# Optimization experiments

Hardware: AMD Instinct MI355X
Metric: run time of the kernel (lower is better)

The kernel has to match this reference:

```python
import jax, jax.numpy as jnp
import numpy as np

NUM_HEADS = 12


def _qkv_split(x, qkv_w, num_heads):
    B, N, C = x.shape
    hd = C // num_heads
    qkv = (x @ qkv_w).reshape(B, N, 3, num_heads, hd)
    qkv = jnp.transpose(qkv, (2, 0, 3, 1, 4))  # [3, B, H, N, hd]
    return qkv[0], qkv[1], qkv[2]


def setup_inputs() -> dict:
    key = jax.random.key(0)
    k1, k2, k3, k4 = jax.random.split(key, 4)
    B, N, C = 8, 1024, 768
    s = 0.02
    return {
        "x1": jax.random.normal(k1, (B, N, C), dtype=jnp.float32),
        "x2": jax.random.normal(k2, (B, N, C), dtype=jnp.float32),
        "qkv_w": jax.random.normal(k3, (C, 3 * C), dtype=jnp.float32) * s,
        "proj_w": jax.random.normal(k4, (C, C), dtype=jnp.float32) * s,
        "proj_b": jnp.zeros((C,), dtype=jnp.float32),
    }


def reference(x1, x2, qkv_w, proj_w, proj_b):
    B, N, C = x1.shape
    H = NUM_HEADS
    hd = C // H
    scale = hd ** (-0.5)

    q, k, v = _qkv_split(x1, qkv_w, H)    # each [B, H, N, hd]
    q2, k2, v2 = _qkv_split(x2, qkv_w, H)

    # self-attention branch: q attends to k/v (from x1)
    attn1 = jax.nn.softmax(jnp.einsum('bhqd,bhkd->bhqk', q, k) * scale, axis=-1)
    o1 = jnp.einsum('bhqk,bhkd->bhqd', attn1, v)

    # cross-attention branch: same q attends to k2/v2 (from x2)
    attn2 = jax.nn.softmax(jnp.einsum('bhqd,bhkd->bhqk', q, k2) * scale, axis=-1)
    o2 = jnp.einsum('bhqk,bhkd->bhqd', attn2, v2)

    o1 = jnp.transpose(o1, (0, 2, 1, 3)).reshape(B, N, C) @ proj_w + proj_b
    o2 = jnp.transpose(o2, (0, 2, 1, 3)).reshape(B, N, C) @ proj_w + proj_b
    return (o1, o2)
```

## Files before the change

kernel.cpp:

```cpp
#include <hip/hip_runtime.h>
#include <hip/hip_bf16.h>

#define N_ 1024
#define C_ 768
#define H_ 12

typedef unsigned short u16;
typedef __attribute__((ext_vector_type(8))) short bf16x8;
typedef __attribute__((ext_vector_type(4))) float f32x4;
typedef __attribute__((ext_vector_type(16))) float f32x16;

#define MFMA16(a, b, c) __builtin_amdgcn_mfma_f32_16x16x32_bf16(a, b, c, 0, 0, 0)
#define MFMA32(a, b, c) __builtin_amdgcn_mfma_f32_32x32x16_bf16(a, b, c, 0, 0, 0)

#define GLDS16(gp, lp) __builtin_amdgcn_global_load_lds(                     \
    (const __attribute__((address_space(1))) void*)(gp),                     \
    (__attribute__((address_space(3))) void*)(lp), 16, 0, 0)

__device__ __forceinline__ u16 f2bu(float x) {
    unsigned u = __float_as_uint(x);
    unsigned r = (u + 0x7fffu + ((u >> 16) & 1u)) >> 16;
    return (u16)r;
}

__device__ __forceinline__ unsigned cvtpk(float a, float b) {
    unsigned d;
    asm("v_cvt_pk_bf16_f32 %0, %1, %2" : "=v"(d) : "v"(a), "v"(b));
    return d;
}

__global__ __launch_bounds__(256) void cvt_x(
    const float* __restrict__ x1, const float* __restrict__ x2,
    u16* __restrict__ d1, u16* __restrict__ d2)
{
    const size_t G = 786432;
    for (size_t i = (size_t)blockIdx.x * 256 + threadIdx.x; i < 2 * G;
         i += (size_t)gridDim.x * 256) {
        const float* src = (i < G) ? x1 : x2;
        u16* dst = (i < G) ? d1 : d2;
        size_t g = (i < G) ? i : i - G;
        float4 f0 = ((const float4*)src)[g * 2];
        float4 f1 = ((const float4*)src)[g * 2 + 1];
        ushort4 lo, hi;
        lo.x = f2bu(f0.x); lo.y = f2bu(f0.y); lo.z = f2bu(f0.z); lo.w = f2bu(f0.w);
        hi.x = f2bu(f1.x); hi.y = f2bu(f1.y); hi.z = f2bu(f1.z); hi.w = f2bu(f1.w);
        ((ushort4*)dst)[g * 2] = lo;
        ((ushort4*)dst)[g * 2 + 1] = hi;
    }
}

__global__ __launch_bounds__(256) void tr_cvt(
    const float* __restrict__ W, u16* __restrict__ WT, int R, int CC)
{
    __shared__ float t[32][33];
    const int tx = threadIdx.x & 31, ty = threadIdx.x >> 5;
    const int c0 = blockIdx.x * 32, r0 = blockIdx.y * 32;
#pragma unroll
    for (int i = 0; i < 4; ++i) {
        int r = ty + i * 8;
        t[r][tx] = W[(size_t)(r0 + r) * CC + c0 + tx];
    }
    __syncthreads();
#pragma unroll
    for (int i = 0; i < 4; ++i) {
        int c = ty + i * 8;
        WT[(size_t)(c0 + c) * R + r0 + tx] = f2bu(t[tx][c]);
    }
}

__global__ __launch_bounds__(256, 4) void qkv_gemm(
    const u16* __restrict__ A1, const u16* __restrict__ A2,
    const u16* __restrict__ BT, u16* __restrict__ qd,
    u16* __restrict__ k1d, u16* __restrict__ k2d,
    u16* __restrict__ vt1d, u16* __restrict__ vt2d)
{
    __shared__ u16 As[3][128 * 32];
    __shared__ u16 Bs[3][128 * 32];
    const int tid = threadIdx.x;
    const int w = tid >> 6, lane = tid & 63;
    const int c31 = lane & 31, h = lane >> 5;
    const int wm = w >> 1, wn = w & 1;
    const int id = blockIdx.x;
    const int xcd = id & 7, j = id >> 3;
    const int by = xcd * 8 + j / 30;
    const int bx = j % 30;
    const bool first = bx < 18;
    const u16* A = first ? A1 : A2;
    const int row0 = by * 128;
    const int nc0 = first ? bx * 128 : 768 + (bx - 18) * 128;

    f32x16 acc[2][2];
#pragma unroll
    for (int i = 0; i < 2; ++i)
#pragma unroll
        for (int jj = 0; jj < 2; ++jj)
#pragma unroll
            for (int e = 0; e < 16; ++e) acc[i][jj][e] = 0.f;

    int aoff[2], boff[2];
    char *adst[2], *bdst[2];
#pragma unroll
    for (int i = 0; i < 2; ++i) {
        int L = (i * 256 + tid) * 16;
        int row = L >> 6;
        int slot = (L >> 4) & 3;
        int sw = (slot ^ ((row >> 1) & 3)) * 8;
        aoff[i] = (row0 + row) * C_ + sw;
        boff[i] = (nc0 + row) * C_ + sw;
        adst[i] = (char*)&As[0][0] + i * 4096 + w * 1024;
        bdst[i] = (char*)&Bs[0][0] + i * 4096 + w * 1024;
    }
    auto stage = [&](int buf, int k0) {
#pragma unroll
        for (int i = 0; i < 2; ++i) {
            GLDS16(A + aoff[i] + k0, adst[i] + buf * 8192);
            GLDS16(BT + boff[i] + k0, bdst[i] + buf * 8192);
        }
    };

    const int ra0 = wm * 64 + c31, ra1 = ra0 + 32;
    const int rb0 = wn * 64 + c31, rb1 = rb0 + 32;

    stage(0, 0);
    stage(1, 32);
    int buf = 0;
    for (int kt = 0; kt < 24; ++kt) {
        if (kt < 23) { asm volatile("s_waitcnt vmcnt(4)" ::: "memory"); }
        else         { asm volatile("s_waitcnt vmcnt(0)" ::: "memory"); }
        __builtin_amdgcn_s_barrier();
        if (kt + 2 < 24) {
            int nb = buf + 2; if (nb >= 3) nb -= 3;
            stage(nb, (kt + 2) * 32);
        }
        const char* abase = (const char*)&As[0][0] + buf * 8192;
        const char* bbase = (const char*)&Bs[0][0] + buf * 8192;
#pragma unroll
        for (int kh = 0; kh < 2; ++kh) {
            bf16x8 a0 = *(const bf16x8*)(abase + ra0 * 64 + (((h + 2 * kh) ^ ((ra0 >> 1) & 3)) * 16));
            bf16x8 a1 = *(const bf16x8*)(abase + ra1 * 64 + (((h + 2 * kh) ^ ((ra1 >> 1) & 3)) * 16));
            bf16x8 b0 = *(const bf16x8*)(bbase + rb0 * 64 + (((h + 2 * kh) ^ ((rb0 >> 1) & 3)) * 16));
            bf16x8 b1 = *(const bf16x8*)(bbase + rb1 * 64 + (((h + 2 * kh) ^ ((rb1 >> 1) & 3)) * 16));
            acc[0][0] = MFMA32(a0, b0, acc[0][0]);
            acc[0][1] = MFMA32(a0, b1, acc[0][1]);
            acc[1][0] = MFMA32(a1, b0, acc[1][0]);
            acc[1][1] = MFMA32(a1, b1, acc[1][1]);
        }
        if (++buf >= 3) buf = 0;
    }

    u16* kd  = first ? k1d : k2d;
    u16* vtd = first ? vt1d : vt2d;
    const int abscol = nc0 + wn * 64;
    const int sec = abscol / C_;
    const int hh = (abscol % C_) >> 6;
    const float scl = (sec == 0) ? 0.180336877f : 1.0f;
#pragma unroll
    for (int mt = 0; mt < 2; ++mt)
#pragma unroll
        for (int nt = 0; nt < 2; ++nt)
#pragma unroll
            for (int r = 0; r < 16; ++r) {
                int row = row0 + wm * 64 + mt * 32 + (r & 3) + 8 * (r >> 2) + 4 * h;
                int b = row >> 10, n = row & 1023;
                int d = nt * 32 + c31;
                u16 val = f2bu(acc[mt][nt][r] * scl);
                size_t bh = (size_t)(b * H_ + hh);
                if (sec == 0)      qd[(bh * N_ + n) * 64 + d] = val;
                else if (sec == 1) kd[(bh * N_ + n) * 64 + d] = val;
                else {
                    int nprm = (n & ~63) | (((n & 15) << 2) | ((n >> 4) & 3));
                    vtd[(bh * 64 + d) * N_ + nprm] = val;
                }
            }
}

__global__ __launch_bounds__(256, 4) void proj_gemm(
    const u16* __restrict__ A1, const u16* __restrict__ A2,
    const u16* __restrict__ BT, const float* __restrict__ bias,
    float* __restrict__ out)
{
    __shared__ u16 As[3][128 * 32];
    __shared__ u16 Bs[3][128 * 32];
    const int tid = threadIdx.x;
    const int w = tid >> 6, lane = tid & 63;
    const int c31 = lane & 31, h = lane >> 5;
    const int wm = w >> 1, wn = w & 1;
    const int sel = blockIdx.y >> 6;
    const u16* A = sel ? A2 : A1;
    float* op = out + (size_t)sel * 8192 * C_;
    const int row0 = (blockIdx.y & 63) * 128;
    const int nc0 = blockIdx.x * 128;

    f32x16 acc[2][2];
#pragma unroll
    for (int i = 0; i < 2; ++i)
#pragma unroll
        for (int jj = 0; jj < 2; ++jj)
#pragma unroll
            for (int e = 0; e < 16; ++e) acc[i][jj][e] = 0.f;

    int aoff[2], boff[2];
    char *adst[2], *bdst[2];
#pragma unroll
    for (int i = 0; i < 2; ++i) {
        int L = (i * 256 + tid) * 16;
        int row = L >> 6;
        int slot = (L >> 4) & 3;
        int sw = (slot ^ ((row >> 1) & 3)) * 8;
        aoff[i] = (row0 + row) * C_ + sw;
        boff[i] = (nc0 + row) * C_ + sw;
        adst[i] = (char*)&As[0][0] + i * 4096 + w * 1024;
        bdst[i] = (char*)&Bs[0][0] + i * 4096 + w * 1024;
    }
    auto stage = [&](int buf, int k0) {
#pragma unroll
        for (int i = 0; i < 2; ++i) {
            GLDS16(A + aoff[i] + k0, adst[i] + buf * 8192);
            GLDS16(BT + boff[i] + k0, bdst[i] + buf * 8192);
        }
    };

    const int ra0 = wm * 64 + c31, ra1 = ra0 + 32;
    const int rb0 = wn * 64 + c31, rb1 = rb0 + 32;

    stage(0, 0);
    stage(1, 32);
    int buf = 0;
    for (int kt = 0; kt < 24; ++kt) {
        if (kt < 23) { asm volatile("s_waitcnt vmcnt(4)" ::: "memory"); }
        else         { asm volatile("s_waitcnt vmcnt(0)" ::: "memory"); }
        __builtin_amdgcn_s_barrier();
        if (kt + 2 < 24) {
            int nb = buf + 2; if (nb >= 3) nb -= 3;
            stage(nb, (kt + 2) * 32);
        }
        const char* abase = (const char*)&As[0][0] + buf * 8192;
        const char* bbase = (const char*)&Bs[0][0] + buf * 8192;
#pragma unroll
        for (int kh = 0; kh < 2; ++kh) {
            bf16x8 a0 = *(const bf16x8*)(abase + ra0 * 64 + (((h + 2 * kh) ^ ((ra0 >> 1) & 3)) * 16));
            bf16x8 a1 = *(const bf16x8*)(abase + ra1 * 64 + (((h + 2 * kh) ^ ((ra1 >> 1) & 3)) * 16));
            bf16x8 b0 = *(const bf16x8*)(bbase + rb0 * 64 + (((h + 2 * kh) ^ ((rb0 >> 1) & 3)) * 16));
            bf16x8 b1 = *(const bf16x8*)(bbase + rb1 * 64 + (((h + 2 * kh) ^ ((rb1 >> 1) & 3)) * 16));
            acc[0][0] = MFMA32(a0, b0, acc[0][0]);
            acc[0][1] = MFMA32(a0, b1, acc[0][1]);
            acc[1][0] = MFMA32(a1, b0, acc[1][0]);
            acc[1][1] = MFMA32(a1, b1, acc[1][1]);
        }
        if (++buf >= 3) buf = 0;
    }

#pragma unroll
    for (int mt = 0; mt < 2; ++mt)
#pragma unroll
        for (int nt = 0; nt < 2; ++nt)
#pragma unroll
            for (int r = 0; r < 16; ++r) {
                int row = row0 + wm * 64 + mt * 32 + (r & 3) + 8 * (r >> 2) + 4 * h;
                int col = nc0 + wn * 64 + nt * 32 + c31;
                op[(size_t)row * C_ + col] = acc[mt][nt][r] + bias[col];
            }
}

__global__ __launch_bounds__(256) void attn_mfma(
    const u16* __restrict__ Q,
    const u16* __restrict__ K1, const u16* __restrict__ VT1,
    const u16* __restrict__ K2, const u16* __restrict__ VT2,
    u16* __restrict__ O1, u16* __restrict__ O2)
{
    __shared__ u16 Ks[2][64 * 64];
    __shared__ u16 Vs[2][64 * 64];
    __shared__ u16 Ps[4][32 * 72];
    const int tid = threadIdx.x;
    const int w = tid >> 6, lane = tid & 63;
    const int g = lane >> 4, ln = lane & 15;
    const int id = blockIdx.x;
    const int xcd = id & 7, j = id >> 3;
    const int unit = j >> 3;
    const int qb = j & 7;
    const int br = unit >= 12;
    const int bh = xcd * 12 + (br ? unit - 12 : unit);
    const int qw = qb * 128 + w * 32;
    const size_t hb = (size_t)bh * N_ * 64;

    const u16* Kb = (br ? K2 : K1) + hb;
    const u16* Vb = (br ? VT2 : VT1) + hb;
    const u16* Qb = Q + hb;
    u16* O        = br ? O2 : O1;

    bf16x8 qf[2][2];
#pragma unroll
    for (int mt = 0; mt < 2; ++mt)
#pragma unroll
        for (int s = 0; s < 2; ++s)
            qf[mt][s] = *(const bf16x8*)(Qb + (size_t)(qw + mt * 16 + ln) * 64 + s * 32 + g * 8);

    f32x4 o[2][4];
    float lsum[2][4];
#pragma unroll
    for (int mt = 0; mt < 2; ++mt) {
#pragma unroll
        for (int t = 0; t < 4; ++t) o[mt][t] = (f32x4){0.f, 0.f, 0.f, 0.f};
#pragma unroll
        for (int r = 0; r < 4; ++r) lsum[mt][r] = 0.f;
    }

    auto stage = [&](int buf, int key0) {
#pragma unroll
        for (int i = 0; i < 2; ++i) {
            int L = (i * 256 + tid) * 16;
            int row = L >> 7;
            int sw = (((L >> 4) & 7) ^ (row & 7)) * 8;
            GLDS16(Kb + (size_t)(key0 + row) * 64 + sw,
                   (char*)&Ks[buf][0] + i * 4096 + w * 1024);
            GLDS16(Vb + (size_t)row * N_ + key0 + sw,
                   (char*)&Vs[buf][0] + i * 4096 + w * 1024);
        }
    };

    u16* pw = &Ps[w][0];
    const int r7 = ln & 7;

    stage(0, 0);
    __syncthreads();
    for (int kt = 0; kt < 16; ++kt) {
        const int buf = kt & 1;
        if (kt < 15) stage(buf ^ 1, (kt + 1) * 64);
        const char* kbase = (const char*)&Ks[buf][0];
        f32x4 st[2][4];
#pragma unroll
        for (int nt = 0; nt < 4; ++nt) {
            const char* krow = kbase + (nt * 16 + ln) * 128;
            bf16x8 kf0 = *(const bf16x8*)(krow + ((g ^ r7) * 16));
            bf16x8 kf1 = *(const bf16x8*)(krow + (((g + 4) ^ r7) * 16));
#pragma unroll
            for (int mt = 0; mt < 2; ++mt) {
                f32x4 z = (f32x4){0.f, 0.f, 0.f, 0.f};
                z = MFMA16(qf[mt][0], kf0, z);
                z = MFMA16(qf[mt][1], kf1, z);
                st[mt][nt] = z;
            }
        }
#pragma unroll
        for (int mt = 0; mt < 2; ++mt)
#pragma unroll
            for (int r = 0; r < 4; ++r) {
                float p0 = __builtin_amdgcn_exp2f(st[mt][0][r]);
                float p1 = __builtin_amdgcn_exp2f(st[mt][1][r]);
                float p2 = __builtin_amdgcn_exp2f(st[mt][2][r]);
                float p3 = __builtin_amdgcn_exp2f(st[mt][3][r]);
                lsum[mt][r] += (p0 + p1) + (p2 + p3);
                uint2 pk;
                pk.x = cvtpk(p0, p1);
                pk.y = cvtpk(p2, p3);
                int prow = mt * 16 + g * 4 + r;
                *(uint2*)((char*)pw + prow * 144 + ln * 8) = pk;
            }
        const char* vbase = (const char*)&Vs[buf][0];
#pragma unroll
        for (int s = 0; s < 2; ++s) {
            bf16x8 pa[2];
            pa[0] = *(const bf16x8*)((const char*)pw + (0 + ln) * 144 + s * 64 + g * 16);
            pa[1] = *(const bf16x8*)((const char*)pw + (16 + ln) * 144 + s * 64 + g * 16);
#pragma unroll
            for (int t = 0; t < 4; ++t) {
                bf16x8 vf = *(const bf16x8*)(vbase + (t * 16 + ln) * 128 + (((s * 4 + g) ^ r7) * 16));
#pragma unroll
                for (int mt = 0; mt < 2; ++mt) o[mt][t] = MFMA16(pa[mt], vf, o[mt][t]);
            }
        }
        __syncthreads();
    }
    const int b = bh / H_, h = bh % H_;
#pragma unroll
    for (int mt = 0; mt < 2; ++mt)
#pragma unroll
        for (int r = 0; r < 4; ++r) {
            float ls = lsum[mt][r];
#pragma unroll
            for (int off = 8; off; off >>= 1) ls += __shfl_xor(ls, off);
            float inv = 1.f / ls;
            int n = qw + mt * 16 + g * 4 + r;
            u16* orow = O + ((size_t)(b * N_) + n) * C_ + h * 64 + ln;
#pragma unroll
            for (int t = 0; t < 4; ++t)
                orow[t * 16] = f2bu(o[mt][t][r] * inv);
        }
}

extern "C" void kernel_launch(void* const* d_in, const int* in_sizes, int n_in,
                              void* d_out, int out_size, void* d_ws, size_t ws_size,
                              hipStream_t stream) {
    const float* x1     = (const float*)d_in[0];
    const float* x2     = (const float*)d_in[1];
    const float* qkv_w  = (const float*)d_in[2];
    const float* proj_w = (const float*)d_in[3];
    const float* proj_b = (const float*)d_in[4];
    float* out = (float*)d_out;

    u16* ws = (u16*)d_ws;
    const size_t SZ = (size_t)8 * H_ * N_ * 64;
    u16* wqkvT  = ws;
    u16* wprojT = wqkvT + (size_t)2304 * 768;
    u16* q      = wprojT + (size_t)768 * 768;
    u16* k1     = q + SZ;
    u16* vT1    = k1 + SZ;
    u16* slotA  = vT1 + SZ;
    u16* vT2    = slotA + SZ;
    u16* slotB  = vT2 + SZ;
    u16* x1c = slotA, *o2p = slotA;
    u16* x2c = slotB, *o1p = slotB;
    u16* k2buf = (u16*)(out + SZ);

    cvt_x<<<2048, 256, 0, stream>>>(x1, x2, x1c, x2c);
    tr_cvt<<<dim3(72, 24), 256, 0, stream>>>(qkv_w, wqkvT, C_, 3 * C_);
    tr_cvt<<<dim3(24, 24), 256, 0, stream>>>(proj_w, wprojT, C_, C_);
    qkv_gemm<<<1920, 256, 0, stream>>>(x1c, x2c, wqkvT, q, k1, k2buf, vT1, vT2);
    attn_mfma<<<1536, 256, 0, stream>>>(q, k1, vT1, k2buf, vT2, o1p, o2p);
    proj_gemm<<<dim3(6, 128), 256, 0, stream>>>(o1p, o2p, wprojT, proj_b, out);
}
```

Measured before the change: 222.2 us.

## Switch QKV and proj GEMMs to BK=64 double-buffered LDS pipeline

Both GEMM kernels move from a triple-buffered K=32 tile pipeline to a double-buffered K=64 pipeline. Each iteration issues the next stage before waiting and adds a second barrier after compute, with a new 8-way XOR swizzle over 128-byte rows. The aim is to halve the loop trip count and barrier overhead per unit of work. LDS per block grows from 48KB to 64KB and the min-blocks hint is dropped, which can lower occupancy.

```diff
diff --git a/kernel.cpp b/kernel.cpp
--- a/kernel.cpp
+++ b/kernel.cpp
@@ -68,14 +68,14 @@
     }
 }
 
-__global__ __launch_bounds__(256, 4) void qkv_gemm(
+__global__ __launch_bounds__(256) void qkv_gemm(
     const u16* __restrict__ A1, const u16* __restrict__ A2,
     const u16* __restrict__ BT, u16* __restrict__ qd,
     u16* __restrict__ k1d, u16* __restrict__ k2d,
     u16* __restrict__ vt1d, u16* __restrict__ vt2d)
 {
-    __shared__ u16 As[3][128 * 32];
-    __shared__ u16 Bs[3][128 * 32];
+    __shared__ u16 As[2][128 * 64];
+    __shared__ u16 Bs[2][128 * 64];
     const int tid = threadIdx.x;
     const int w = tid >> 6, lane = tid & 63;
     const int c31 = lane & 31, h = lane >> 5;
@@ -97,24 +97,24 @@
 #pragma unroll
             for (int e = 0; e < 16; ++e) acc[i][jj][e] = 0.f;
 
-    int aoff[2], boff[2];
-    char *adst[2], *bdst[2];
-#pragma unroll
-    for (int i = 0; i < 2; ++i) {
-        int L = (i * 256 + tid) * 16;
-        int row = L >> 6;
-        int slot = (L >> 4) & 3;
-        int sw = (slot ^ ((row >> 1) & 3)) * 8;
-        aoff[i] = (row0 + row) * C_ + sw;
-        boff[i] = (nc0 + row) * C_ + sw;
-        adst[i] = (char*)&As[0][0] + i * 4096 + w * 1024;
-        bdst[i] = (char*)&Bs[0][0] + i * 4096 + w * 1024;
-    }
+    int aoff[4], boff[4];
+    {
+        const int srow = tid >> 3;
+        const int sch = ((tid & 7) ^ (srow & 7)) * 8;
+#pragma unroll
+        for (int i = 0; i < 4; ++i) {
+            int row = i * 32 + srow;
+            aoff[i] = (row0 + row) * C_ + sch;
+            boff[i] = (nc0 + row) * C_ + sch;
+        }
+    }
+    char* adst0 = (char*)&As[0][0] + w * 1024;
+    char* bdst0 = (char*)&Bs[0][0] + w * 1024;
     auto stage = [&](int buf, int k0) {
 #pragma unroll
-        for (int i = 0; i < 2; ++i) {
-            GLDS16(A + aoff[i] + k0, adst[i] + buf * 8192);
-            GLDS16(BT + boff[i] + k0, bdst[i] + buf * 8192);
+        for (int i = 0; i < 4; ++i) {
+            GLDS16(A + aoff[i] + k0, adst0 + buf * 16384 + i * 4096);
+            GLDS16(BT + boff[i] + k0, bdst0 + buf * 16384 + i * 4096);
         }
     };
 
@@ -122,30 +122,30 @@
     const int rb0 = wn * 64 + c31, rb1 = rb0 + 32;
 
     stage(0, 0);
-    stage(1, 32);
-    int buf = 0;
-    for (int kt = 0; kt < 24; ++kt) {
-        if (kt < 23) { asm volatile("s_waitcnt vmcnt(4)" ::: "memory"); }
-        else         { asm volatile("s_waitcnt vmcnt(0)" ::: "memory"); }
+    for (int kt = 0; kt < 12; ++kt) {
+        const int buf = kt & 1;
+        if (kt < 11) {
+            stage(buf ^ 1, (kt + 1) * 64);
+            asm volatile("s_waitcnt vmcnt(8)" ::: "memory");
+        } else {
+            asm volatile("s_waitcnt vmcnt(0)" ::: "memory");
+        }
         __builtin_amdgcn_s_barrier();
-        if (kt + 2 < 24) {
-            int nb = buf + 2; if (nb >= 3) nb -= 3;
-            stage(nb, (kt + 2) * 32);
-        }
-        const char* abase = (const char*)&As[0][0] + buf * 8192;
-        const char* bbase = (const char*)&Bs[0][0] + buf * 8192;
-#pragma unroll
-        for (int kh = 0; kh < 2; ++kh) {
-            bf16x8 a0 = *(const bf16x8*)(abase + ra0 * 64 + (((h + 2 * kh) ^ ((ra0 >> 1) & 3)) * 16));
-            bf16x8 a1 = *(const bf16x8*)(abase + ra1 * 64 + (((h + 2 * kh) ^ ((ra1 >> 1) & 3)) * 16));
-            bf16x8 b0 = *(const bf16x8*)(bbase + rb0 * 64 + (((h + 2 * kh) ^ ((rb0 >> 1) & 3)) * 16));
-            bf16x8 b1 = *(const bf16x8*)(bbase + rb1 * 64 + (((h + 2 * kh) ^ ((rb1 >> 1) & 3)) * 16));
+        const char* abase = (const char*)&As[0][0] + buf * 16384;
+        const char* bbase = (const char*)&Bs[0][0] + buf * 16384;
+#pragma unroll
+        for (int kh = 0; kh < 4; ++kh) {
+            bf16x8 a0 = *(const bf16x8*)(abase + ra0 * 128 + (((2 * kh + h) ^ (ra0 & 7)) * 16));
+            bf16x8 a1 = *(const bf16x8*)(abase + ra1 * 128 + (((2 * kh + h) ^ (ra1 & 7)) * 16));
+            bf16x8 b0 = *(const bf16x8*)(bbase + rb0 * 128 + (((2 * kh + h) ^ (rb0 & 7)) * 16));
+            bf16x8 b1 = *(const bf16x8*)(bbase + rb1 * 128 + (((2 * kh + h) ^ (rb1 & 7)) * 16));
             acc[0][0] = MFMA32(a0, b0, acc[0][0]);
             acc[0][1] = MFMA32(a0, b1, acc[0][1]);
             acc[1][0] = MFMA32(a1, b0, acc[1][0]);
             acc[1][1] = MFMA32(a1, b1, acc[1][1]);
         }
-        if (++buf >= 3) buf = 0;
+        asm volatile("" ::: "memory");
+        __builtin_amdgcn_s_barrier();
     }
 
     u16* kd  = first ? k1d : k2d;
@@ -174,13 +174,13 @@
             }
 }
 
-__global__ __launch_bounds__(256, 4) void proj_gemm(
+__global__ __launch_bounds__(256) void proj_gemm(
     const u16* __restrict__ A1, const u16* __restrict__ A2,
     const u16* __restrict__ BT, const float* __restrict__ bias,
     float* __restrict__ out)
 {
-    __shared__ u16 As[3][128 * 32];
-    __shared__ u16 Bs[3][128 * 32];
+    __shared__ u16 As[2][128 * 64];
+    __shared__ u16 Bs[2][128 * 64];
     const int tid = threadIdx.x;
     const int w = tid >> 6, lane = tid & 63;
     const int c31 = lane & 31, h = lane >> 5;
@@ -199,24 +199,24 @@
 #pragma unroll
             for (int e = 0; e < 16; ++e) acc[i][jj][e] = 0.f;
 
-    int aoff[2], boff[2];
-    char *adst[2], *bdst[2];
-#pragma unroll
-    for (int i = 0; i < 2; ++i) {
-        int L = (i * 256 + tid) * 16;
-        int row = L >> 6;
-        int slot = (L >> 4) & 3;
-        int sw = (slot ^ ((row >> 1) & 3)) * 8;
-        aoff[i] = (row0 + row) * C_ + sw;
-        boff[i] = (nc0 + row) * C_ + sw;
-        adst[i] = (char*)&As[0][0] + i * 4096 + w * 1024;
-        bdst[i] = (char*)&Bs[0][0] + i * 4096 + w * 1024;
-    }
+    int aoff[4], boff[4];
+    {
+        const int srow = tid >> 3;
+        const int sch = ((tid & 7) ^ (srow & 7)) * 8;
+#pragma unroll
+        for (int i = 0; i < 4; ++i) {
+            int row = i * 32 + srow;
+            aoff[i] = (row0 + row) * C_ + sch;
+            boff[i] = (nc0 + row) * C_ + sch;
+        }
+    }
+    char* adst0 = (char*)&As[0][0] + w * 1024;
+    char* bdst0 = (char*)&Bs[0][0] + w * 1024;
     auto stage = [&](int buf, int k0) {
 #pragma unroll
-        for (int i = 0; i < 2; ++i) {
-            GLDS16(A + aoff[i] + k0, adst[i] + buf * 8192);
-            GLDS16(BT + boff[i] + k0, bdst[i] + buf * 8192);
+        for (int i = 0; i < 4; ++i) {
+            GLDS16(A + aoff[i] + k0, adst0 + buf * 16384 + i * 4096);
+            GLDS16(BT + boff[i] + k0, bdst0 + buf * 16384 + i * 4096);
         }
     };
 
@@ -224,30 +224,30 @@
     const int rb0 = wn * 64 + c31, rb1 = rb0 + 32;
 
     stage(0, 0);
-    stage(1, 32);
-    int buf = 0;
-    for (int kt = 0; kt < 24; ++kt) {
-        if (kt < 23) { asm volatile("s_waitcnt vmcnt(4)" ::: "memory"); }
-        else         { asm volatile("s_waitcnt vmcnt(0)" ::: "memory"); }
+    for (int kt = 0; kt < 12; ++kt) {
+        const int buf = kt & 1;
+        if (kt < 11) {
+            stage(buf ^ 1, (kt + 1) * 64);
+            asm volatile("s_waitcnt vmcnt(8)" ::: "memory");
+        } else {
+            asm volatile("s_waitcnt vmcnt(0)" ::: "memory");
+        }
         __builtin_amdgcn_s_barrier();
-        if (kt + 2 < 24) {
-            int nb = buf + 2; if (nb >= 3) nb -= 3;
-            stage(nb, (kt + 2) * 32);
-        }
-        const char* abase = (const char*)&As[0][0] + buf * 8192;
-        const char* bbase = (const char*)&Bs[0][0] + buf * 8192;
-#pragma unroll
-        for (int kh = 0; kh < 2; ++kh) {
-            bf16x8 a0 = *(const bf16x8*)(abase + ra0 * 64 + (((h + 2 * kh) ^ ((ra0 >> 1) & 3)) * 16));
-            bf16x8 a1 = *(const bf16x8*)(abase + ra1 * 64 + (((h + 2 * kh) ^ ((ra1 >> 1) & 3)) * 16));
-            bf16x8 b0 = *(const bf16x8*)(bbase + rb0 * 64 + (((h + 2 * kh) ^ ((rb0 >> 1) & 3)) * 16));
-            bf16x8 b1 = *(const bf16x8*)(bbase + rb1 * 64 + (((h + 2 * kh) ^ ((rb1 >> 1) & 3)) * 16));
+        const char* abase = (const char*)&As[0][0] + buf * 16384;
+        const char* bbase = (const char*)&Bs[0][0] + buf * 16384;
+#pragma unroll
+        for (int kh = 0; kh < 4; ++kh) {
+            bf16x8 a0 = *(const bf16x8*)(abase + ra0 * 128 + (((2 * kh + h) ^ (ra0 & 7)) * 16));
+            bf16x8 a1 = *(const bf16x8*)(abase + ra1 * 128 + (((2 * kh + h) ^ (ra1 & 7)) * 16));
+            bf16x8 b0 = *(const bf16x8*)(bbase + rb0 * 128 + (((2 * kh + h) ^ (rb0 & 7)) * 16));
+            bf16x8 b1 = *(const bf16x8*)(bbase + rb1 * 128 + (((2 * kh + h) ^ (rb1 & 7)) * 16));
             acc[0][0] = MFMA32(a0, b0, acc[0][0]);
             acc[0][1] = MFMA32(a0, b1, acc[0][1]);
             acc[1][0] = MFMA32(a1, b0, acc[1][0]);
             acc[1][1] = MFMA32(a1, b1, acc[1][1]);
         }
-        if (++buf >= 3) buf = 0;
+        asm volatile("" ::: "memory");
+        __builtin_amdgcn_s_barrier();
     }
 
 #pragma unroll
```

New measurement: 217.1 us. 2.3% less time.
